# Kernel tuning notes

Measured on AMD Instinct MI355X. Metric: run time of the kernel, lower is better.

## Reference

```python
import jax, jax.numpy as jnp
import numpy as np

EMBED = 1024
HEADS = 16
HEAD_DIM = EMBED // HEADS
OUT = 1024


def setup_inputs() -> dict:
    key = jax.random.key(0)
    ks = jax.random.split(key, 6)
    x = jax.random.normal(ks[0], (4, 2048, EMBED), dtype=jnp.float32)
    # per-head projection weights, torch Linear convention: [out_features, in_features]
    s = 1.0 / np.sqrt(HEAD_DIM)
    Wv = jax.random.uniform(ks[1], (HEAD_DIM, HEAD_DIM), jnp.float32, -s, s)
    Wk = jax.random.uniform(ks[2], (HEAD_DIM, HEAD_DIM), jnp.float32, -s, s)
    Wq = jax.random.uniform(ks[3], (HEAD_DIM, HEAD_DIM), jnp.float32, -s, s)
    so = 1.0 / np.sqrt(EMBED)
    Wo = jax.random.uniform(ks[4], (OUT, EMBED), jnp.float32, -so, so)
    bo = jax.random.uniform(ks[5], (OUT,), jnp.float32, -so, so)
    return {"x": x, "Wq": Wq, "Wk": Wk, "Wv": Wv, "Wo": Wo, "bo": bo}


def reference(x, Wq, Wk, Wv, Wo, bo):
    N, L, _ = x.shape
    xh = x.reshape(N, L, HEADS, HEAD_DIM)  # nqhd
    q = jnp.einsum('nqhd,ed->nqhe', xh, Wq)
    k = jnp.einsum('nkhd,ed->nkhe', xh, Wk)
    v = jnp.einsum('nkhd,ed->nkhe', xh, Wv)
    # full score matrix [N, H, Q, K], scaled by sqrt(embed_size) as in source
    energy = jnp.einsum('nqhd,nkhd->nhqk', q, k) / np.sqrt(EMBED).astype(np.float32)
    attn = jax.nn.softmax(energy, axis=3)
    out = jnp.einsum('nhqk,nkhd->nqhd', attn, v).reshape(N, L, EMBED)
    return out @ Wo.T + bo
```

## Files before the change

### kernel.cpp

```cpp
#include <hip/hip_runtime.h>
#include <hip/hip_bf16.h>
#include <stdint.h>
#include <stddef.h>


typedef __attribute__((ext_vector_type(8))) short bf16x8;
typedef __attribute__((ext_vector_type(4))) float f32x4;
typedef __attribute__((ext_vector_type(4))) short short4v;
typedef __attribute__((ext_vector_type(2))) uint32_t uint2v;

__device__ __forceinline__ f32x4 mfma16(bf16x8 a, bf16x8 b, f32x4 c) {
    return __builtin_amdgcn_mfma_f32_16x16x32_bf16(a, b, c, 0, 0, 0);
}

__device__ __forceinline__ short f2bf(float x) {
    union { float f; uint32_t u; } v; v.f = x;
    uint32_t r = (v.u + 0x7FFFu + ((v.u >> 16) & 1u)) >> 16;
    return (short)(uint16_t)r;
}

__device__ __forceinline__ uint32_t pk2bf(float a, float b) {
    union { __hip_bfloat162 h; uint32_t u; } v;
    v.h = __float22bfloat162_rn(float2{a, b});
    return v.u;
}

__device__ __forceinline__ bf16x8 cvt8(const float* __restrict__ p) {
    f32x4 a = *(const f32x4*)p;
    f32x4 b = *(const f32x4*)(p + 4);
    bf16x8 r;
    r[0] = f2bf(a[0]); r[1] = f2bf(a[1]); r[2] = f2bf(a[2]); r[3] = f2bf(a[3]);
    r[4] = f2bf(b[0]); r[5] = f2bf(b[1]); r[6] = f2bf(b[2]); r[7] = f2bf(b[3]);
    return r;
}

__global__ __launch_bounds__(256)
void wpack_kernel(const float* __restrict__ Wo, const float* __restrict__ Wq,
                  const float* __restrict__ Wk, const float* __restrict__ Wv,
                  short* __restrict__ wo_f, short* __restrict__ wqkv_f) {
    int b = blockIdx.x;
    if (b < 512) {
        int idx = b * 256 + threadIdx.x;
        int nrow = idx >> 7;
        int k0 = (idx & 127) * 8;
        bf16x8 v = cvt8(Wo + (size_t)nrow * 1024 + k0);
        int ntile = nrow >> 4, lcn = nrow & 15;
        int kseg = k0 >> 5, qd = (k0 >> 3) & 3;
        *(bf16x8*)(wo_f + ((size_t)(ntile * 32 + kseg) * 64 + qd * 16 + lcn) * 8) = v;
    } else {
        const float* W = (b == 512) ? Wq : (b == 513) ? Wk : Wv;
        short* dst = wqkv_f + (size_t)(b - 512) * 4096;
        for (int u = threadIdx.x; u < 512; u += 256) {
            int seg = u >> 6, ln = u & 63;
            int nt = seg >> 1, kf = seg & 1, lq = ln >> 4, lcn = ln & 15;
            bf16x8 v = cvt8(W + (nt * 16 + lcn) * 64 + kf * 32 + lq * 8);
            *(bf16x8*)(dst + u * 8) = v;
        }
    }
}

__global__ __launch_bounds__(256)
void kvproj_kernel(const float* __restrict__ x, const short* __restrict__ wqkv_f,
                   short* __restrict__ kf_ws, short* __restrict__ vf_ws) {
    __shared__ alignas(16) short kbuf[128 * 72];
    __shared__ alignas(16) short vbuf[64 * 136];
    int tid = threadIdx.x;
    int lt = blockIdx.x & 15, nh = blockIdx.x >> 4;
    int n = nh >> 4, h = nh & 15;
    int l0 = lt * 128, kt0 = lt * 2;
    int wv = tid >> 6, lane = tid & 63, quad = lane >> 4, lc = lane & 15;
    const short* wkf = wqkv_f + 4096 + lane * 8;
    const short* wvf = wqkv_f + 8192 + lane * 8;

    for (int u = tid; u < 1024; u += 256) {
        int r = u >> 3, c = (u & 7) * 8;
        *(bf16x8*)(kbuf + r * 72 + c) =
            cvt8(x + (size_t)(n * 2048 + l0 + r) * 1024 + h * 64 + c);
    }
    __syncthreads();

    bf16x8 xa[2][2];
    for (int mt = 0; mt < 2; ++mt)
        for (int kf = 0; kf < 2; ++kf)
            xa[mt][kf] = *(bf16x8*)(kbuf + (wv * 32 + mt * 16 + lc) * 72 + kf * 32 + quad * 8);

    f32x4 ka[2][4] = {}, va[2][4] = {};
    for (int nt = 0; nt < 4; ++nt)
        for (int kf = 0; kf < 2; ++kf) {
            bf16x8 wkb = *(const bf16x8*)(wkf + (nt * 2 + kf) * 512);
            bf16x8 wvb = *(const bf16x8*)(wvf + (nt * 2 + kf) * 512);
            for (int mt = 0; mt < 2; ++mt) {
                ka[mt][nt] = mfma16(xa[mt][kf], wkb, ka[mt][nt]);
                va[mt][nt] = mfma16(xa[mt][kf], wvb, va[mt][nt]);
            }
        }

    for (int mt = 0; mt < 2; ++mt) {
        int off = wv * 32 + mt * 16;
        for (int nt = 0; nt < 4; ++nt) {
            short4v pv;
            for (int i = 0; i < 4; ++i) {
                kbuf[(off + quad * 4 + i) * 72 + nt * 16 + lc] = f2bf(ka[mt][nt][i]);
                pv[i] = f2bf(va[mt][nt][i]);
            }
            *(short4v*)(vbuf + (nt * 16 + lc) * 136 + off + quad * 4) = pv;
        }
    }
    __syncthreads();

    size_t base = (size_t)nh * 131072 + (size_t)kt0 * 4096;
    for (int u = tid; u < 1024; u += 256) {
        int tile = u >> 9, rem = u & 511, seg = rem >> 6, ln = u & 63;
        int t = seg >> 1, kf = seg & 1;
        int lq = ln >> 4, ll = ln & 15;
        bf16x8 kw = *(bf16x8*)(kbuf + (tile * 64 + t * 16 + ll) * 72 + kf * 32 + lq * 8);
        *(bf16x8*)(kf_ws + base + (size_t)tile * 4096 + seg * 512 + ln * 8) = kw;
        bf16x8 vw = *(bf16x8*)(vbuf + (t * 16 + ll) * 136 + tile * 64 + kf * 32 + lq * 8);
        *(bf16x8*)(vf_ws + base + (size_t)tile * 4096 + seg * 512 + ln * 8) = vw;
    }
}

__global__ __launch_bounds__(256)
void flash_kernel(const float* __restrict__ x, const short* __restrict__ wqkv_f,
                  const short* __restrict__ kf_ws, const short* __restrict__ vf_ws,
                  short* __restrict__ ao) {
    __shared__ alignas(16) short pbuf[128 * 72];
    int tid = threadIdx.x;
    int nh = blockIdx.x & 63, qt = blockIdx.x >> 6;
    int n = nh >> 4, h = nh & 15;
    int q0 = qt * 128;
    int wv = tid >> 6, lane = tid & 63, quad = lane >> 4, lc = lane & 15;

    for (int u = tid; u < 1024; u += 256) {
        int r = u >> 3, c = (u & 7) * 8;
        *(bf16x8*)(pbuf + r * 72 + c) =
            cvt8(x + (size_t)(n * 2048 + q0 + r) * 1024 + h * 64 + c);
    }
    __syncthreads();
    {
        const short* wqf = wqkv_f + lane * 8;
        bf16x8 xa[2][2];
        for (int mt = 0; mt < 2; ++mt)
            for (int kf = 0; kf < 2; ++kf)
                xa[mt][kf] = *(bf16x8*)(pbuf + (wv * 32 + mt * 16 + lc) * 72 +
                                        kf * 32 + quad * 8);
        f32x4 qacc[2][4] = {};
        for (int nt = 0; nt < 4; ++nt)
            for (int kf = 0; kf < 2; ++kf) {
                bf16x8 wb = *(const bf16x8*)(wqf + (nt * 2 + kf) * 512);
                for (int mt = 0; mt < 2; ++mt)
                    qacc[mt][nt] = mfma16(xa[mt][kf], wb, qacc[mt][nt]);
            }
        const float QS = 0.04508422002778011f;
        for (int mt = 0; mt < 2; ++mt)
            for (int nt = 0; nt < 4; ++nt)
                for (int i = 0; i < 4; ++i)
                    pbuf[(wv * 32 + mt * 16 + quad * 4 + i) * 72 + nt * 16 + lc] =
                        f2bf(qacc[mt][nt][i] * QS);
    }
    bf16x8 qa[2][2];
    for (int mt = 0; mt < 2; ++mt)
        for (int kf = 0; kf < 2; ++kf)
            qa[mt][kf] = *(bf16x8*)(pbuf + (wv * 32 + mt * 16 + lc) * 72 +
                                    kf * 32 + quad * 8);

    f32x4 o[2][4] = {};
    float lsum[2] = {0.f, 0.f};
    const short* kbase = kf_ws + (size_t)nh * 131072 + lane * 8;
    const short* vbase = vf_ws + (size_t)nh * 131072 + lane * 8;

    for (int kt = 0; kt < 32; ++kt) {
        const short* kp = kbase + (size_t)kt * 4096;
        const short* vp = vbase + (size_t)kt * 4096;
        bf16x8 kA[4][2];
#pragma unroll
        for (int t = 0; t < 4; ++t)
            for (int kf = 0; kf < 2; ++kf)
                kA[t][kf] = *(const bf16x8*)(kp + (t * 2 + kf) * 512);
        f32x4 s[2][4] = {};
#pragma unroll
        for (int t = 0; t < 4; ++t)
            for (int q2 = 0; q2 < 2; ++q2) {
                s[q2][t] = mfma16(kA[t][0], qa[q2][0], s[q2][t]);
                s[q2][t] = mfma16(kA[t][1], qa[q2][1], s[q2][t]);
            }
        bf16x8 vA[4][2];
#pragma unroll
        for (int dt = 0; dt < 4; ++dt)
            for (int kf = 0; kf < 2; ++kf)
                vA[dt][kf] = *(const bf16x8*)(vp + (dt * 2 + kf) * 512);
#pragma unroll
        for (int q2 = 0; q2 < 2; ++q2) {
            int prow = (wv * 32 + q2 * 16 + lc) * 72;
            float ts = 0.f;
#pragma unroll
            for (int t = 0; t < 4; ++t) {
                float p0 = __builtin_amdgcn_exp2f(s[q2][t][0]);
                float p1 = __builtin_amdgcn_exp2f(s[q2][t][1]);
                float p2 = __builtin_amdgcn_exp2f(s[q2][t][2]);
                float p3 = __builtin_amdgcn_exp2f(s[q2][t][3]);
                ts += (p0 + p1) + (p2 + p3);
                uint2v w = {pk2bf(p0, p1), pk2bf(p2, p3)};
                *(uint2v*)(pbuf + prow + t * 16 + quad * 4) = w;
            }
            lsum[q2] += ts;
        }
#pragma unroll
        for (int q2 = 0; q2 < 2; ++q2)
            for (int kf = 0; kf < 2; ++kf) {
                bf16x8 pB = *(bf16x8*)(pbuf + (wv * 32 + q2 * 16 + lc) * 72 +
                                       kf * 32 + quad * 8);
                for (int dt = 0; dt < 4; ++dt)
                    o[q2][dt] = mfma16(vA[dt][kf], pB, o[q2][dt]);
            }
    }

    for (int q2 = 0; q2 < 2; ++q2) {
        float t = lsum[q2];
        t += __shfl_xor(t, 16, 64);
        t += __shfl_xor(t, 32, 64);
        float inv = 1.f / t;
        int mtile = (n * 2048 + q0) / 16 + wv * 2 + q2;
        for (int dt = 0; dt < 4; ++dt) {
            int kseg = h * 2 + (dt >> 1);
            int qd8 = ((dt & 1) * 4 + quad) >> 1;
            short4v pk;
            for (int i = 0; i < 4; ++i) pk[i] = f2bf(o[q2][dt][i] * inv);
            *(short4v*)(ao + (size_t)(mtile * 32 + kseg) * 512 +
                        (qd8 * 16 + lc) * 8 + (quad & 1) * 4) = pk;
        }
    }
}

__global__ __launch_bounds__(256)
void outgemm_kernel(const short* __restrict__ afb, const short* __restrict__ wfb,
                    const float* __restrict__ bo, float* __restrict__ out) {
    int tid = threadIdx.x;
    int bm = blockIdx.x & 63, bn = blockIdx.x >> 6;
    int m0 = bm * 128, n0 = bn * 128;
    int wv = tid >> 6, lane = tid & 63, quad = lane >> 4, lc = lane & 15;
    int wr = wv >> 1, wc = wv & 1;
    int mtb = bm * 8 + wr * 4;
    int ntb = bn * 8 + wc * 4;

    const short* ab = afb + lane * 8;
    const short* bb = wfb + lane * 8;

    f32x4 acc[4][4] = {};
    for (int kt = 0; kt < 32; ++kt) {
        bf16x8 af[4], bfr[4];
#pragma unroll
        for (int mt = 0; mt < 4; ++mt)
            af[mt] = *(const bf16x8*)(ab + ((size_t)(mtb + mt) * 32 + kt) * 512);
#pragma unroll
        for (int nt = 0; nt < 4; ++nt)
            bfr[nt] = *(const bf16x8*)(bb + ((size_t)(ntb + nt) * 32 + kt) * 512);
#pragma unroll
        for (int mt = 0; mt < 4; ++mt)
            for (int nt = 0; nt < 4; ++nt)
                acc[mt][nt] = mfma16(af[mt], bfr[nt], acc[mt][nt]);
    }
    for (int nt = 0; nt < 4; ++nt) {
        float bv = bo[n0 + wc * 64 + nt * 16 + lc];
        for (int mt = 0; mt < 4; ++mt)
            for (int i = 0; i < 4; ++i) {
                int m = m0 + wr * 64 + mt * 16 + quad * 4 + i;
                int nn = n0 + wc * 64 + nt * 16 + lc;
                out[(size_t)m * 1024 + nn] = acc[mt][nt][i] + bv;
            }
    }
}

extern "C" void kernel_launch(void* const* d_in, const int* in_sizes, int n_in,
                              void* d_out, int out_size, void* d_ws, size_t ws_size,
                              hipStream_t stream) {
    const float* x  = (const float*)d_in[0];
    const float* Wq = (const float*)d_in[1];
    const float* Wk = (const float*)d_in[2];
    const float* Wv = (const float*)d_in[3];
    const float* Wo = (const float*)d_in[4];
    const float* bo = (const float*)d_in[5];
    float* out = (float*)d_out;

    short* kf_ws   = (short*)d_ws;
    short* vf_ws   = kf_ws + 8388608;
    short* ao_ws   = vf_ws + 8388608;
    short* wo_f    = ao_ws + 8388608;
    short* wqkv_f  = wo_f + 1048576;

    wpack_kernel<<<dim3(515), dim3(256), 0, stream>>>(Wo, Wq, Wk, Wv, wo_f, wqkv_f);
    kvproj_kernel<<<dim3(1024), dim3(256), 0, stream>>>(x, wqkv_f, kf_ws, vf_ws);
    flash_kernel<<<dim3(1024), dim3(256), 0, stream>>>(x, wqkv_f, kf_ws, vf_ws, ao_ws);
    outgemm_kernel<<<dim3(512), dim3(256), 0, stream>>>(ao_ws, wo_f, bo, out);
}
```

Baseline: 220.0 us.

## Double flash query tile to 256 rows to halve K/V reloads per block

Each flash block now handles 256 query rows (64 per wave) instead of 128, so each K/V tile loaded from the workspace is reused across twice as many queries. The grid shrinks from 1024 to 512 blocks. The QK^T stage is also reorganised to load K fragments per key sub-tile and compute scores and exponentials incrementally, which keeps fewer score registers live. The trade-offs are more accumulator registers per thread (o[4][4]), double the shared memory, and fewer blocks to fill the GPU's compute units, so occupancy and tail balance may suffer.

```diff
diff --git a/kernel.cpp b/kernel.cpp
--- a/kernel.cpp
+++ b/kernel.cpp
@@ -120,18 +120,18 @@
     }
 }
 
-__global__ __launch_bounds__(256)
+__global__ __launch_bounds__(256, 2)
 void flash_kernel(const float* __restrict__ x, const short* __restrict__ wqkv_f,
                   const short* __restrict__ kf_ws, const short* __restrict__ vf_ws,
                   short* __restrict__ ao) {
-    __shared__ alignas(16) short pbuf[128 * 72];
+    __shared__ alignas(16) short pbuf[256 * 72];
     int tid = threadIdx.x;
     int nh = blockIdx.x & 63, qt = blockIdx.x >> 6;
     int n = nh >> 4, h = nh & 15;
-    int q0 = qt * 128;
+    int q0 = qt * 256;
     int wv = tid >> 6, lane = tid & 63, quad = lane >> 4, lc = lane & 15;
 
-    for (int u = tid; u < 1024; u += 256) {
+    for (int u = tid; u < 2048; u += 256) {
         int r = u >> 3, c = (u & 7) * 8;
         *(bf16x8*)(pbuf + r * 72 + c) =
             cvt8(x + (size_t)(n * 2048 + q0 + r) * 1024 + h * 64 + c);
@@ -139,88 +139,85 @@
     __syncthreads();
     {
         const short* wqf = wqkv_f + lane * 8;
-        bf16x8 xa[2][2];
-        for (int mt = 0; mt < 2; ++mt)
+        bf16x8 xa[4][2];
+        for (int mt = 0; mt < 4; ++mt)
             for (int kf = 0; kf < 2; ++kf)
-                xa[mt][kf] = *(bf16x8*)(pbuf + (wv * 32 + mt * 16 + lc) * 72 +
+                xa[mt][kf] = *(bf16x8*)(pbuf + (wv * 64 + mt * 16 + lc) * 72 +
                                         kf * 32 + quad * 8);
-        f32x4 qacc[2][4] = {};
+        f32x4 qacc[4][4] = {};
         for (int nt = 0; nt < 4; ++nt)
             for (int kf = 0; kf < 2; ++kf) {
                 bf16x8 wb = *(const bf16x8*)(wqf + (nt * 2 + kf) * 512);
-                for (int mt = 0; mt < 2; ++mt)
+                for (int mt = 0; mt < 4; ++mt)
                     qacc[mt][nt] = mfma16(xa[mt][kf], wb, qacc[mt][nt]);
             }
         const float QS = 0.04508422002778011f;
-        for (int mt = 0; mt < 2; ++mt)
+        for (int mt = 0; mt < 4; ++mt)
             for (int nt = 0; nt < 4; ++nt)
                 for (int i = 0; i < 4; ++i)
-                    pbuf[(wv * 32 + mt * 16 + quad * 4 + i) * 72 + nt * 16 + lc] =
+                    pbuf[(wv * 64 + mt * 16 + quad * 4 + i) * 72 + nt * 16 + lc] =
                         f2bf(qacc[mt][nt][i] * QS);
     }
-    bf16x8 qa[2][2];
-    for (int mt = 0; mt < 2; ++mt)
+    bf16x8 qa[4][2];
+    for (int mt = 0; mt < 4; ++mt)
         for (int kf = 0; kf < 2; ++kf)
-            qa[mt][kf] = *(bf16x8*)(pbuf + (wv * 32 + mt * 16 + lc) * 72 +
+            qa[mt][kf] = *(bf16x8*)(pbuf + (wv * 64 + mt * 16 + lc) * 72 +
                                     kf * 32 + quad * 8);
 
-    f32x4 o[2][4] = {};
-    float lsum[2] = {0.f, 0.f};
+    f32x4 o[4][4] = {};
+    float lsum[4] = {0.f, 0.f, 0.f, 0.f};
     const short* kbase = kf_ws + (size_t)nh * 131072 + lane * 8;
     const short* vbase = vf_ws + (size_t)nh * 131072 + lane * 8;
 
     for (int kt = 0; kt < 32; ++kt) {
         const short* kp = kbase + (size_t)kt * 4096;
         const short* vp = vbase + (size_t)kt * 4096;
-        bf16x8 kA[4][2];
-#pragma unroll
-        for (int t = 0; t < 4; ++t)
-            for (int kf = 0; kf < 2; ++kf)
-                kA[t][kf] = *(const bf16x8*)(kp + (t * 2 + kf) * 512);
-        f32x4 s[2][4] = {};
-#pragma unroll
-        for (int t = 0; t < 4; ++t)
-            for (int q2 = 0; q2 < 2; ++q2) {
-                s[q2][t] = mfma16(kA[t][0], qa[q2][0], s[q2][t]);
-                s[q2][t] = mfma16(kA[t][1], qa[q2][1], s[q2][t]);
-            }
         bf16x8 vA[4][2];
 #pragma unroll
         for (int dt = 0; dt < 4; ++dt)
             for (int kf = 0; kf < 2; ++kf)
                 vA[dt][kf] = *(const bf16x8*)(vp + (dt * 2 + kf) * 512);
-#pragma unroll
-        for (int q2 = 0; q2 < 2; ++q2) {
-            int prow = (wv * 32 + q2 * 16 + lc) * 72;
-            float ts = 0.f;
-#pragma unroll
-            for (int t = 0; t < 4; ++t) {
-                float p0 = __builtin_amdgcn_exp2f(s[q2][t][0]);
-                float p1 = __builtin_amdgcn_exp2f(s[q2][t][1]);
-                float p2 = __builtin_amdgcn_exp2f(s[q2][t][2]);
-                float p3 = __builtin_amdgcn_exp2f(s[q2][t][3]);
-                ts += (p0 + p1) + (p2 + p3);
+
+#pragma unroll
+        for (int t = 0; t < 4; ++t) {
+            bf16x8 k0 = *(const bf16x8*)(kp + (t * 2 + 0) * 512);
+            bf16x8 k1 = *(const bf16x8*)(kp + (t * 2 + 1) * 512);
+            f32x4 s[4];
+#pragma unroll
+            for (int q2 = 0; q2 < 4; ++q2) {
+                f32x4 acc = {};
+                acc = mfma16(k0, qa[q2][0], acc);
+                acc = mfma16(k1, qa[q2][1], acc);
+                s[q2] = acc;
+            }
+#pragma unroll
+            for (int q2 = 0; q2 < 4; ++q2) {
+                float p0 = __builtin_amdgcn_exp2f(s[q2][0]);
+                float p1 = __builtin_amdgcn_exp2f(s[q2][1]);
+                float p2 = __builtin_amdgcn_exp2f(s[q2][2]);
+                float p3 = __builtin_amdgcn_exp2f(s[q2][3]);
+                lsum[q2] += (p0 + p1) + (p2 + p3);
                 uint2v w = {pk2bf(p0, p1), pk2bf(p2, p3)};
-                *(uint2v*)(pbuf + prow + t * 16 + quad * 4) = w;
-            }
-            lsum[q2] += ts;
-        }
-#pragma unroll
-        for (int q2 = 0; q2 < 2; ++q2)
+                *(uint2v*)(pbuf + (wv * 64 + q2 * 16 + lc) * 72 + t * 16 + quad * 4) = w;
+            }
+        }
+
+#pragma unroll
+        for (int q2 = 0; q2 < 4; ++q2)
             for (int kf = 0; kf < 2; ++kf) {
-                bf16x8 pB = *(bf16x8*)(pbuf + (wv * 32 + q2 * 16 + lc) * 72 +
+                bf16x8 pB = *(bf16x8*)(pbuf + (wv * 64 + q2 * 16 + lc) * 72 +
                                        kf * 32 + quad * 8);
                 for (int dt = 0; dt < 4; ++dt)
                     o[q2][dt] = mfma16(vA[dt][kf], pB, o[q2][dt]);
             }
     }
 
-    for (int q2 = 0; q2 < 2; ++q2) {
+    for (int q2 = 0; q2 < 4; ++q2) {
         float t = lsum[q2];
         t += __shfl_xor(t, 16, 64);
         t += __shfl_xor(t, 32, 64);
         float inv = 1.f / t;
-        int mtile = (n * 2048 + q0) / 16 + wv * 2 + q2;
+        int mtile = (n * 2048 + q0) / 16 + wv * 4 + q2;
         for (int dt = 0; dt < 4; ++dt) {
             int kseg = h * 2 + (dt >> 1);
             int qd8 = ((dt & 1) * 4 + quad) >> 1;
@@ -290,6 +287,6 @@
 
     wpack_kernel<<<dim3(515), dim3(256), 0, stream>>>(Wo, Wq, Wk, Wv, wo_f, wqkv_f);
     kvproj_kernel<<<dim3(1024), dim3(256), 0, stream>>>(x, wqkv_f, kf_ws, vf_ws);
-    flash_kernel<<<dim3(1024), dim3(256), 0, stream>>>(x, wqkv_f, kf_ws, vf_ws, ao_ws);
+    flash_kernel<<<dim3(512), dim3(256), 0, stream>>>(x, wqkv_f, kf_ws, vf_ws, ao_ws);
     outgemm_kernel<<<dim3(512), dim3(256), 0, stream>>>(ao_ws, wo_f, bo, out);
 }
```

Result: no change. 217.3 us (-1.2%).
